# Kernel tuning notes

Hardware: AMD Instinct MI355X
Metric: run time of the kernel (lower is better)

Reference implementation:

```python
import jax, jax.numpy as jnp
import numpy as np

N_NODES = 50000
BN_EPS = 1e-5


def setup_inputs() -> dict:
    key = jax.random.key(0)
    ks = jax.random.split(key, 10)
    n, e, d, L = N_NODES, 500000, 128, 2
    x = jax.random.normal(ks[0], (n, d), dtype=jnp.float32)
    edge_index = jax.random.randint(ks[1], (2, e), 0, n, dtype=jnp.int64)
    edge_attr = jax.random.normal(ks[2], (e, d), dtype=jnp.float32)
    W1 = jax.random.normal(ks[3], (L, d, d), dtype=jnp.float32) * 0.05
    b1 = jax.random.normal(ks[4], (L, d), dtype=jnp.float32) * 0.02
    gamma = 1.0 + 0.1 * jax.random.normal(ks[5], (L, d), dtype=jnp.float32)
    beta = 0.1 * jax.random.normal(ks[6], (L, d), dtype=jnp.float32)
    W2 = jax.random.normal(ks[7], (L, d, d), dtype=jnp.float32) * 0.05
    b2 = jax.random.normal(ks[8], (L, d), dtype=jnp.float32) * 0.02
    return {"x": x, "edge_index": edge_index, "edge_attr": edge_attr,
            "W1": W1, "b1": b1, "gamma": gamma, "beta": beta, "W2": W2, "b2": b2}


def _gine_layer(x, src, dst, edge_attr, W1l, b1l, gl, bl, W2l, b2l):
    # GINEConv message: relu(x_j + edge_attr), sum-aggregated to target nodes
    msg = jax.nn.relu(x[src] + edge_attr)              # [E, d]
    agg = jax.ops.segment_sum(msg, dst, num_segments=N_NODES)  # [N, d]
    h = (x + agg) @ W1l + b1l                           # eps=0 -> (1+eps)*x = x
    # BatchNorm1d over nodes (train-mode batch stats, biased var)
    mu = jnp.mean(h, axis=0)
    var = jnp.mean(jnp.square(h - mu), axis=0)
    h = (h - mu) * jax.lax.rsqrt(var + BN_EPS) * gl + bl
    h = jax.nn.relu(h)
    h = jax.nn.relu(h @ W2l + b2l)
    return jax.nn.relu(h)  # encoder's outer activation


def reference(x, edge_index, edge_attr, W1, b1, gamma, beta, W2, b2):
    src, dst = edge_index[0], edge_index[1]
    L = W1.shape[0]
    for l in range(L):
        x = _gine_layer(x, src, dst, edge_attr, W1[l], b1[l], gamma[l], beta[l], W2[l], b2[l])
    return x
```

## Files before the change

kernel.cpp:

```cpp
#include <hip/hip_runtime.h>

#define BN_EPS 1e-5f

using f4 = __attribute__((ext_vector_type(4))) float;
using h4 = __attribute__((ext_vector_type(4))) _Float16;

__device__ inline f4 relu4(f4 v) {
    v.x = fmaxf(v.x, 0.f); v.y = fmaxf(v.y, 0.f);
    v.z = fmaxf(v.z, 0.f); v.w = fmaxf(v.w, 0.f);
    return v;
}

__global__ __launch_bounds__(256) void detect_i64_kernel(const int* __restrict__ ei,
                                                         int* __restrict__ flag, int npairs,
                                                         int* __restrict__ deg, int N) {
    __shared__ int ok;
    if (threadIdx.x == 0) ok = 1;
    __syncthreads();
    bool bad = false;
    for (int i = threadIdx.x; i < npairs; i += 256)
        bad |= (ei[2 * i + 1] != 0);
    if (bad) ok = 0;
    int nq = N >> 2;
    int4* d4 = (int4*)deg;
    for (int i = threadIdx.x; i < nq; i += 256) d4[i] = make_int4(0, 0, 0, 0);
    for (int i = (nq << 2) + threadIdx.x; i < N; i += 256) deg[i] = 0;
    __syncthreads();
    if (threadIdx.x == 0) *flag = ok;
}

__global__ __launch_bounds__(256) void canon_kernel(const int* __restrict__ ei,
                                                    const int* __restrict__ flag,
                                                    int* __restrict__ canon,
                                                    int* __restrict__ deg, int n2, int E) {
    int i = blockIdx.x * 256 + threadIdx.x;
    if (i >= n2) return;
    int wide = *flag;
    int v = wide ? ei[2 * i] : ei[i];
    canon[i] = v;
    if (i >= E) atomicAdd(&deg[v], 1);
}

__global__ __launch_bounds__(256) void scan_blk_kernel(const int* __restrict__ deg,
                                                       int* __restrict__ rowptr,
                                                       int* __restrict__ partials, int N) {
    __shared__ int s[256];
    int b = blockIdx.x, t = threadIdx.x;
    int base = b * 1024 + t * 4;
    int4 v = make_int4(0, 0, 0, 0);
    if (base + 3 < N) v = *(const int4*)(deg + base);
    else {
        if (base < N) v.x = deg[base];
        if (base + 1 < N) v.y = deg[base + 1];
        if (base + 2 < N) v.z = deg[base + 2];
        if (base + 3 < N) v.w = deg[base + 3];
    }
    s[t] = v.x + v.y + v.z + v.w;
    __syncthreads();
    for (int off = 1; off < 256; off <<= 1) {
        int u = (t >= off) ? s[t - off] : 0;
        __syncthreads();
        s[t] += u;
        __syncthreads();
    }
    int excl = (t == 0) ? 0 : s[t - 1];
    int4 w;
    w.x = excl;
    w.y = excl + v.x;
    w.z = w.y + v.y;
    w.w = w.z + v.z;
    if (base + 3 < N) *(int4*)(rowptr + base) = w;
    else {
        if (base < N) rowptr[base] = w.x;
        if (base + 1 < N) rowptr[base + 1] = w.y;
        if (base + 2 < N) rowptr[base + 2] = w.z;
        if (base + 3 < N) rowptr[base + 3] = w.w;
    }
    if (t == 255) partials[b] = s[255];
}

__global__ __launch_bounds__(256) void scan_part_kernel(int* __restrict__ partials, int nb) {
    __shared__ int s[256];
    int t = threadIdx.x;
    if (nb <= 256) {
        s[t] = (t < nb) ? partials[t] : 0;
        __syncthreads();
        for (int off = 1; off < 256; off <<= 1) {
            int u = (t >= off) ? s[t - off] : 0;
            __syncthreads();
            s[t] += u;
            __syncthreads();
        }
        if (t < nb) partials[t] = (t == 0) ? 0 : s[t - 1];
    } else if (t == 0) {
        int run = 0;
        for (int i = 0; i < nb; ++i) { int d = partials[i]; partials[i] = run; run += d; }
    }
}

__global__ __launch_bounds__(256) void scan_add_kernel(int* __restrict__ rowptr,
                                                       int* __restrict__ cursor,
                                                       const int* __restrict__ partials,
                                                       float* __restrict__ sums, int nsum,
                                                       int N, int E) {
    int i = blockIdx.x * 256 + threadIdx.x;
    if (i < nsum) sums[i] = 0.f;
    if (i < N) {
        int v = rowptr[i] + partials[i >> 10];
        rowptr[i] = v;
        cursor[i] = v;
    }
    if (i == N) rowptr[N] = E;
}

__global__ __launch_bounds__(256) void fill_kernel(const int* __restrict__ src,
                                                   const int* __restrict__ dst,
                                                   int* __restrict__ cursor,
                                                   int2* __restrict__ pbuf, int E) {
    int e = blockIdx.x * 256 + threadIdx.x;
    if (e >= E) return;
    int d = dst[e];
    int pos = atomicAdd(&cursor[d], 1);
    pbuf[pos] = make_int2(e, src[e]);
}

template <int MODE>
__global__ __launch_bounds__(256) void gather_kernel(const float* __restrict__ x,
                                                     const float* __restrict__ ea,
                                                     _Float16* __restrict__ eah,
                                                     const int* __restrict__ rowptr,
                                                     const int2* __restrict__ pbuf,
                                                     float* __restrict__ aggx, int N) {
    int t = blockIdx.x * 256 + threadIdx.x;
    int n = t >> 5;
    if (n >= N) return;
    int f = t & 31;
    int lo = rowptr[n], hi = rowptr[n + 1];
    f4 acc0 = ((const f4*)(x + (size_t)n * 128))[f];
    f4 acc1 = {0.f, 0.f, 0.f, 0.f};
    f4 acc2 = {0.f, 0.f, 0.f, 0.f};
    f4 acc3 = {0.f, 0.f, 0.f, 0.f};
    int i = lo;
    if (MODE == 1) {
        const h4* ep = (const h4*)eah;
        for (; i + 4 <= hi; i += 4) {
            int2 q0 = pbuf[i];
            int2 q1 = pbuf[i + 1];
            int2 q2 = pbuf[i + 2];
            int2 q3 = pbuf[i + 3];
            f4 xa = ((const f4*)(x + (size_t)q0.y * 128))[f];
            h4 ha = ep[(size_t)i * 32 + f];
            f4 xb = ((const f4*)(x + (size_t)q1.y * 128))[f];
            h4 hb = ep[(size_t)(i + 1) * 32 + f];
            f4 xc = ((const f4*)(x + (size_t)q2.y * 128))[f];
            h4 hc = ep[(size_t)(i + 2) * 32 + f];
            f4 xd = ((const f4*)(x + (size_t)q3.y * 128))[f];
            h4 hd = ep[(size_t)(i + 3) * 32 + f];
            acc0 += relu4(xa + __builtin_convertvector(ha, f4));
            acc1 += relu4(xb + __builtin_convertvector(hb, f4));
            acc2 += relu4(xc + __builtin_convertvector(hc, f4));
            acc3 += relu4(xd + __builtin_convertvector(hd, f4));
        }
        for (; i < hi; ++i) {
            int2 q0 = pbuf[i];
            f4 xa = ((const f4*)(x + (size_t)q0.y * 128))[f];
            h4 ha = ep[(size_t)i * 32 + f];
            acc0 += relu4(xa + __builtin_convertvector(ha, f4));
        }
    } else {
        h4* ep = (h4*)eah;
        for (; i + 4 <= hi; i += 4) {
            int2 q0 = pbuf[i];
            int2 q1 = pbuf[i + 1];
            int2 q2 = pbuf[i + 2];
            int2 q3 = pbuf[i + 3];
            f4 xa = ((const f4*)(x + (size_t)q0.y * 128))[f];
            f4 aa = __builtin_nontemporal_load(((const f4*)(ea + (size_t)q0.x * 128)) + f);
            f4 xb = ((const f4*)(x + (size_t)q1.y * 128))[f];
            f4 ab = __builtin_nontemporal_load(((const f4*)(ea + (size_t)q1.x * 128)) + f);
            f4 xc = ((const f4*)(x + (size_t)q2.y * 128))[f];
            f4 ac = __builtin_nontemporal_load(((const f4*)(ea + (size_t)q2.x * 128)) + f);
            f4 xd = ((const f4*)(x + (size_t)q3.y * 128))[f];
            f4 ad = __builtin_nontemporal_load(((const f4*)(ea + (size_t)q3.x * 128)) + f);
            if (MODE == 0) {
                ep[(size_t)i * 32 + f] = __builtin_convertvector(aa, h4);
                ep[(size_t)(i + 1) * 32 + f] = __builtin_convertvector(ab, h4);
                ep[(size_t)(i + 2) * 32 + f] = __builtin_convertvector(ac, h4);
                ep[(size_t)(i + 3) * 32 + f] = __builtin_convertvector(ad, h4);
            }
            acc0 += relu4(xa + aa);
            acc1 += relu4(xb + ab);
            acc2 += relu4(xc + ac);
            acc3 += relu4(xd + ad);
        }
        for (; i < hi; ++i) {
            int2 q0 = pbuf[i];
            f4 xa = ((const f4*)(x + (size_t)q0.y * 128))[f];
            f4 aa = __builtin_nontemporal_load(((const f4*)(ea + (size_t)q0.x * 128)) + f);
            if (MODE == 0) ep[(size_t)i * 32 + f] = __builtin_convertvector(aa, h4);
            acc0 += relu4(xa + aa);
        }
    }
    f4 r = (acc0 + acc1) + (acc2 + acc3);
    ((f4*)(aggx + (size_t)n * 128))[f] = r;
}

__global__ __launch_bounds__(256) void gemm1_kernel(const float* A,
                                                    const float* __restrict__ W,
                                                    const float* __restrict__ bias,
                                                    float* __restrict__ sums,
                                                    float* out, int N) {
    __shared__ float sA[64][132];
    __shared__ float sW[32][128];
    int t = threadIdx.x;
    int rbase = blockIdx.x * 64;

    {
        int colq = t & 31;
        int r0 = t >> 5;
#pragma unroll
        for (int it = 0; it < 8; ++it) {
            int r = r0 + it * 8;
            int row = rbase + r;
            float4 v = make_float4(0.f, 0.f, 0.f, 0.f);
            if (row < N) v = reinterpret_cast<const float4*>(A + (size_t)row * 128)[colq];
            *reinterpret_cast<float4*>(&sA[r][colq * 4]) = v;
        }
    }

    float acc[4][8];
#pragma unroll
    for (int r = 0; r < 4; ++r)
#pragma unroll
        for (int c = 0; c < 8; ++c) acc[r][c] = 0.f;

    int cg = t & 15, rg = t >> 4;
    int c0a = cg * 4;
    int c0b = 64 + cg * 4;

    for (int kc = 0; kc < 4; ++kc) {
        __syncthreads();
#pragma unroll
        for (int pass = 0; pass < 4; ++pass) {
            int kk = (t >> 5) + pass * 8;
            int k = kc * 32 + kk;
            float4 w = reinterpret_cast<const float4*>(W + (size_t)k * 128)[t & 31];
            *reinterpret_cast<float4*>(&sW[kk][(t & 31) * 4]) = w;
        }
        __syncthreads();
#pragma unroll
        for (int kk0 = 0; kk0 < 32; kk0 += 4) {
            float4 a[4];
#pragma unroll
            for (int r = 0; r < 4; ++r)
                a[r] = *reinterpret_cast<const float4*>(&sA[rg * 4 + r][kc * 32 + kk0]);
#pragma unroll
            for (int j = 0; j < 4; ++j) {
                float4 w0 = *reinterpret_cast<const float4*>(&sW[kk0 + j][c0a]);
                float4 w1 = *reinterpret_cast<const float4*>(&sW[kk0 + j][c0b]);
#pragma unroll
                for (int r = 0; r < 4; ++r) {
                    float av = (j == 0) ? a[r].x : (j == 1) ? a[r].y : (j == 2) ? a[r].z : a[r].w;
                    acc[r][0] += av * w0.x;
                    acc[r][1] += av * w0.y;
                    acc[r][2] += av * w0.z;
                    acc[r][3] += av * w0.w;
                    acc[r][4] += av * w1.x;
                    acc[r][5] += av * w1.y;
                    acc[r][6] += av * w1.z;
                    acc[r][7] += av * w1.w;
                }
            }
        }
    }

    float4 b0 = *reinterpret_cast<const float4*>(bias + c0a);
    float4 b1v = *reinterpret_cast<const float4*>(bias + c0b);
    float cs[8], cs2[8];
#pragma unroll
    for (int j = 0; j < 8; ++j) { cs[j] = 0.f; cs2[j] = 0.f; }

#pragma unroll
    for (int r = 0; r < 4; ++r) {
        int row = rbase + rg * 4 + r;
        if (row >= N) continue;
        float4 o0, o1;
        o0.x = acc[r][0] + b0.x;  o0.y = acc[r][1] + b0.y;
        o0.z = acc[r][2] + b0.z;  o0.w = acc[r][3] + b0.w;
        o1.x = acc[r][4] + b1v.x; o1.y = acc[r][5] + b1v.y;
        o1.z = acc[r][6] + b1v.z; o1.w = acc[r][7] + b1v.w;
        cs[0] += o0.x; cs2[0] += o0.x * o0.x;
        cs[1] += o0.y; cs2[1] += o0.y * o0.y;
        cs[2] += o0.z; cs2[2] += o0.z * o0.z;
        cs[3] += o0.w; cs2[3] += o0.w * o0.w;
        cs[4] += o1.x; cs2[4] += o1.x * o1.x;
        cs[5] += o1.y; cs2[5] += o1.y * o1.y;
        cs[6] += o1.z; cs2[6] += o1.z * o1.z;
        cs[7] += o1.w; cs2[7] += o1.w * o1.w;
        *reinterpret_cast<float4*>(out + (size_t)row * 128 + c0a) = o0;
        *reinterpret_cast<float4*>(out + (size_t)row * 128 + c0b) = o1;
    }

    __syncthreads();
    float* red = &sA[0][0];
    float* red2 = red + 2048;
    int base = (rg * 16 + cg) * 8;
#pragma unroll
    for (int j = 0; j < 8; ++j) { red[base + j] = cs[j]; red2[base + j] = cs2[j]; }
    __syncthreads();
    if (t < 128) {
        int cgj = (t & 63) >> 2;
        int j = (t & 3) + ((t >> 6) << 2);
        float s = 0.f, s2 = 0.f;
#pragma unroll
        for (int rr = 0; rr < 16; ++rr) {
            s += red[(rr * 16 + cgj) * 8 + j];
            s2 += red2[(rr * 16 + cgj) * 8 + j];
        }
        unsafeAtomicAdd(&sums[t], s);
        unsafeAtomicAdd(&sums[128 + t], s2);
    }
}

__global__ __launch_bounds__(256) void gemm2_kernel(const float* __restrict__ A,
                                                    const float* __restrict__ W,
                                                    const float* __restrict__ bias,
                                                    const float* __restrict__ sums,
                                                    const float* __restrict__ gamma,
                                                    const float* __restrict__ beta,
                                                    float* __restrict__ out, int N,
                                                    float invN) {
    __shared__ float sA[64][132];
    __shared__ float sW[32][128];
    __shared__ float sScale[128];
    __shared__ float sShift[128];
    int t = threadIdx.x;
    int rbase = blockIdx.x * 64;

    if (t < 128) {
        float mean = sums[t] * invN;
        float var = sums[128 + t] * invN - mean * mean;
        float inv = rsqrtf(var + BN_EPS);
        float sc = gamma[t] * inv;
        sScale[t] = sc;
        sShift[t] = beta[t] - mean * sc;
    }
    __syncthreads();

    {
        int colq = t & 31;
        int r0 = t >> 5;
        float4 s4 = reinterpret_cast<const float4*>(sScale)[colq];
        float4 sh4 = reinterpret_cast<const float4*>(sShift)[colq];
#pragma unroll
        for (int it = 0; it < 8; ++it) {
            int r = r0 + it * 8;
            int row = rbase + r;
            float4 v = make_float4(0.f, 0.f, 0.f, 0.f);
            if (row < N) {
                float4 a = reinterpret_cast<const float4*>(A + (size_t)row * 128)[colq];
                v.x = fmaxf(a.x * s4.x + sh4.x, 0.f);
                v.y = fmaxf(a.y * s4.y + sh4.y, 0.f);
                v.z = fmaxf(a.z * s4.z + sh4.z, 0.f);
                v.w = fmaxf(a.w * s4.w + sh4.w, 0.f);
            }
            *reinterpret_cast<float4*>(&sA[r][colq * 4]) = v;
        }
    }

    float acc[4][8];
#pragma unroll
    for (int r = 0; r < 4; ++r)
#pragma unroll
        for (int c = 0; c < 8; ++c) acc[r][c] = 0.f;

    int cg = t & 15, rg = t >> 4;
    int c0a = cg * 4;
    int c0b = 64 + cg * 4;

    for (int kc = 0; kc < 4; ++kc) {
        __syncthreads();
#pragma unroll
        for (int pass = 0; pass < 4; ++pass) {
            int kk = (t >> 5) + pass * 8;
            int k = kc * 32 + kk;
            float4 w = reinterpret_cast<const float4*>(W + (size_t)k * 128)[t & 31];
            *reinterpret_cast<float4*>(&sW[kk][(t & 31) * 4]) = w;
        }
        __syncthreads();
#pragma unroll
        for (int kk0 = 0; kk0 < 32; kk0 += 4) {
            float4 a[4];
#pragma unroll
            for (int r = 0; r < 4; ++r)
                a[r] = *reinterpret_cast<const float4*>(&sA[rg * 4 + r][kc * 32 + kk0]);
#pragma unroll
            for (int j = 0; j < 4; ++j) {
                float4 w0 = *reinterpret_cast<const float4*>(&sW[kk0 + j][c0a]);
                float4 w1 = *reinterpret_cast<const float4*>(&sW[kk0 + j][c0b]);
#pragma unroll
                for (int r = 0; r < 4; ++r) {
                    float av = (j == 0) ? a[r].x : (j == 1) ? a[r].y : (j == 2) ? a[r].z : a[r].w;
                    acc[r][0] += av * w0.x;
                    acc[r][1] += av * w0.y;
                    acc[r][2] += av * w0.z;
                    acc[r][3] += av * w0.w;
                    acc[r][4] += av * w1.x;
                    acc[r][5] += av * w1.y;
                    acc[r][6] += av * w1.z;
                    acc[r][7] += av * w1.w;
                }
            }
        }
    }

    float4 b0 = *reinterpret_cast<const float4*>(bias + c0a);
    float4 b1v = *reinterpret_cast<const float4*>(bias + c0b);
#pragma unroll
    for (int r = 0; r < 4; ++r) {
        int row = rbase + rg * 4 + r;
        if (row >= N) continue;
        float4 o0, o1;
        o0.x = fmaxf(acc[r][0] + b0.x, 0.f);  o0.y = fmaxf(acc[r][1] + b0.y, 0.f);
        o0.z = fmaxf(acc[r][2] + b0.z, 0.f);  o0.w = fmaxf(acc[r][3] + b0.w, 0.f);
        o1.x = fmaxf(acc[r][4] + b1v.x, 0.f); o1.y = fmaxf(acc[r][5] + b1v.y, 0.f);
        o1.z = fmaxf(acc[r][6] + b1v.z, 0.f); o1.w = fmaxf(acc[r][7] + b1v.w, 0.f);
        *reinterpret_cast<float4*>(out + (size_t)row * 128 + c0a) = o0;
        *reinterpret_cast<float4*>(out + (size_t)row * 128 + c0b) = o1;
    }
}

extern "C" void kernel_launch(void* const* d_in, const int* in_sizes, int n_in,
                              void* d_out, int out_size, void* d_ws, size_t ws_size,
                              hipStream_t stream) {
    const float* x     = (const float*)d_in[0];
    const int*   ei    = (const int*)d_in[1];
    const float* ea    = (const float*)d_in[2];
    const float* W1    = (const float*)d_in[3];
    const float* b1    = (const float*)d_in[4];
    const float* gamma = (const float*)d_in[5];
    const float* beta  = (const float*)d_in[6];
    const float* W2    = (const float*)d_in[7];
    const float* b2    = (const float*)d_in[8];

    int N = in_sizes[0] / 128;
    int E = in_sizes[2] / 128;
    int L = in_sizes[3] / (128 * 128);

    size_t NF = (size_t)N * 128;
    float*     buf    = (float*)d_ws;
    float*     sums   = buf + NF;
    _Float16*  eah    = (_Float16*)(sums + 256 * L);
    int*       canon  = (int*)(eah + (size_t)E * 128);
    int*       deg    = canon + (size_t)2 * E;
    int*       rowptr = deg + N;
    int*       cursor = rowptr + N + 2;
    int2*      pbuf   = (int2*)(cursor + N);
    int*       partials = (int*)(pbuf + E);
    int*       flag   = partials + ((N + 1023) / 1024) + 1;

    int npairs = (E < 4096) ? E : 4096;
    detect_i64_kernel<<<1, 256, 0, stream>>>(ei, flag, npairs, deg, N);
    int E2 = 2 * E;
    canon_kernel<<<(E2 + 255) / 256, 256, 0, stream>>>(ei, flag, canon, deg, E2, E);
    const int* src = canon;
    const int* dst = canon + E;

    int nb = (N + 1023) / 1024;
    scan_blk_kernel<<<nb, 256, 0, stream>>>(deg, rowptr, partials, N);
    scan_part_kernel<<<1, 256, 0, stream>>>(partials, nb);
    scan_add_kernel<<<(N + 256) / 256, 256, 0, stream>>>(rowptr, cursor, partials,
                                                         sums, 256 * L, N, E);
    int eBlocks = (E + 255) / 256;
    fill_kernel<<<eBlocks, 256, 0, stream>>>(src, dst, cursor, pbuf, E);

    int gatherBlocks = (N * 32 + 255) / 256;
    int gemmBlocks = (N + 63) / 64;
    float invN = 1.0f / (float)N;
    const float* xin = x;
    for (int l = 0; l < L; ++l) {
        float* xout = (float*)d_out;
        float* sums_l = sums + (size_t)l * 256;
        if (l == 0) {
            if (L > 1)
                gather_kernel<0><<<gatherBlocks, 256, 0, stream>>>(xin, ea, eah, rowptr,
                                                                   pbuf, buf, N);
            else
                gather_kernel<2><<<gatherBlocks, 256, 0, stream>>>(xin, ea, eah, rowptr,
                                                                   pbuf, buf, N);
        } else {
            gather_kernel<1><<<gatherBlocks, 256, 0, stream>>>(xin, ea, eah, rowptr,
                                                               pbuf, buf, N);
        }
        gemm1_kernel<<<gemmBlocks, 256, 0, stream>>>(buf, W1 + (size_t)l * 16384,
                                                     b1 + (size_t)l * 128, sums_l, buf, N);
        gemm2_kernel<<<gemmBlocks, 256, 0, stream>>>(buf, W2 + (size_t)l * 16384,
                                                     b2 + (size_t)l * 128, sums_l,
                                                     gamma + (size_t)l * 128,
                                                     beta + (size_t)l * 128, xout, N, invN);
        xin = xout;
    }
}
```

Measured before the change: 673.3 us.

## Fuse all preprocessing and layer stages into one cooperative persistent megakernel

```diff
diff --git a/kernel.cpp b/kernel.cpp
--- a/kernel.cpp
+++ b/kernel.cpp
@@ -1,4 +1,7 @@
 #include <hip/hip_runtime.h>
+#include <hip/hip_cooperative_groups.h>
+
+namespace cg = cooperative_groups;
 
 #define BN_EPS 1e-5f
 
@@ -11,300 +14,278 @@
     return v;
 }
 
-__global__ __launch_bounds__(256) void detect_i64_kernel(const int* __restrict__ ei,
-                                                         int* __restrict__ flag, int npairs,
-                                                         int* __restrict__ deg, int N) {
-    __shared__ int ok;
-    if (threadIdx.x == 0) ok = 1;
-    __syncthreads();
+struct MegaParams {
+    const float* x; const int* ei; const float* ea;
+    const float* W1; const float* b1; const float* gamma; const float* beta;
+    const float* W2; const float* b2;
+    float* out; float* buf; float* sums; _Float16* eah;
+    int* canon; int* deg; int* rowptr; int* cursor; int2* pbuf;
+    int* partials; int* flag;
+    int N, E, L, npairs;
+};
+
+__device__ inline void dev_init(int* deg, float* sums, int* flag,
+                                int N, int nsum, int gsize, int gtid) {
+    for (int i = gtid; i < N; i += gsize) deg[i] = 0;
+    for (int i = gtid; i < nsum; i += gsize) sums[i] = 0.f;
+    if (gtid == 0) *flag = 1;
+}
+
+__device__ inline void dev_detect(const int* ei, int* flag, int npairs,
+                                  int gsize, int gtid) {
     bool bad = false;
-    for (int i = threadIdx.x; i < npairs; i += 256)
-        bad |= (ei[2 * i + 1] != 0);
-    if (bad) ok = 0;
-    int nq = N >> 2;
-    int4* d4 = (int4*)deg;
-    for (int i = threadIdx.x; i < nq; i += 256) d4[i] = make_int4(0, 0, 0, 0);
-    for (int i = (nq << 2) + threadIdx.x; i < N; i += 256) deg[i] = 0;
-    __syncthreads();
-    if (threadIdx.x == 0) *flag = ok;
-}
-
-__global__ __launch_bounds__(256) void canon_kernel(const int* __restrict__ ei,
-                                                    const int* __restrict__ flag,
-                                                    int* __restrict__ canon,
-                                                    int* __restrict__ deg, int n2, int E) {
-    int i = blockIdx.x * 256 + threadIdx.x;
-    if (i >= n2) return;
+    for (int i = gtid; i < npairs; i += gsize) bad |= (ei[2 * i + 1] != 0);
+    if (bad) atomicAnd(flag, 0);
+}
+
+__device__ inline void dev_canon(const int* ei, const int* flag, int* canon,
+                                 int* deg, int n2, int E, int gsize, int gtid) {
     int wide = *flag;
-    int v = wide ? ei[2 * i] : ei[i];
-    canon[i] = v;
-    if (i >= E) atomicAdd(&deg[v], 1);
-}
-
-__global__ __launch_bounds__(256) void scan_blk_kernel(const int* __restrict__ deg,
-                                                       int* __restrict__ rowptr,
-                                                       int* __restrict__ partials, int N) {
-    __shared__ int s[256];
-    int b = blockIdx.x, t = threadIdx.x;
-    int base = b * 1024 + t * 4;
-    int4 v = make_int4(0, 0, 0, 0);
-    if (base + 3 < N) v = *(const int4*)(deg + base);
-    else {
-        if (base < N) v.x = deg[base];
-        if (base + 1 < N) v.y = deg[base + 1];
-        if (base + 2 < N) v.z = deg[base + 2];
-        if (base + 3 < N) v.w = deg[base + 3];
-    }
-    s[t] = v.x + v.y + v.z + v.w;
-    __syncthreads();
-    for (int off = 1; off < 256; off <<= 1) {
-        int u = (t >= off) ? s[t - off] : 0;
+    for (int i = gtid; i < n2; i += gsize) {
+        int v = wide ? ei[2 * i] : ei[i];
+        canon[i] = v;
+        if (i >= E) atomicAdd(deg + v, 1);
+    }
+}
+
+__device__ inline void dev_scan_local(const int* deg, int* rowptr, int* partials,
+                                      int N, int* sInt) {
+    int t = threadIdx.x;
+    int nchunks = (N + 1023) >> 10;
+    for (int c = blockIdx.x; c < (int)nchunks; c += gridDim.x) {
+        int base = (c << 10) + t * 4;
+        int4 v = make_int4(0, 0, 0, 0);
+        if (base + 3 < N) v = *(const int4*)(deg + base);
+        else {
+            if (base < N) v.x = deg[base];
+            if (base + 1 < N) v.y = deg[base + 1];
+            if (base + 2 < N) v.z = deg[base + 2];
+            if (base + 3 < N) v.w = deg[base + 3];
+        }
+        int s = v.x + v.y + v.z + v.w;
         __syncthreads();
-        s[t] += u;
-        __syncthreads();
-    }
-    int excl = (t == 0) ? 0 : s[t - 1];
-    int4 w;
-    w.x = excl;
-    w.y = excl + v.x;
-    w.z = w.y + v.y;
-    w.w = w.z + v.z;
-    if (base + 3 < N) *(int4*)(rowptr + base) = w;
-    else {
-        if (base < N) rowptr[base] = w.x;
-        if (base + 1 < N) rowptr[base + 1] = w.y;
-        if (base + 2 < N) rowptr[base + 2] = w.z;
-        if (base + 3 < N) rowptr[base + 3] = w.w;
-    }
-    if (t == 255) partials[b] = s[255];
-}
-
-__global__ __launch_bounds__(256) void scan_part_kernel(int* __restrict__ partials, int nb) {
-    __shared__ int s[256];
-    int t = threadIdx.x;
-    if (nb <= 256) {
-        s[t] = (t < nb) ? partials[t] : 0;
+        sInt[t] = s;
         __syncthreads();
         for (int off = 1; off < 256; off <<= 1) {
-            int u = (t >= off) ? s[t - off] : 0;
+            int u = (t >= off) ? sInt[t - off] : 0;
             __syncthreads();
-            s[t] += u;
+            sInt[t] += u;
             __syncthreads();
         }
-        if (t < nb) partials[t] = (t == 0) ? 0 : s[t - 1];
-    } else if (t == 0) {
+        int excl = (t == 0) ? 0 : sInt[t - 1];
+        int4 w;
+        w.x = excl;
+        w.y = excl + v.x;
+        w.z = w.y + v.y;
+        w.w = w.z + v.z;
+        if (base + 3 < N) *(int4*)(rowptr + base) = w;
+        else {
+            if (base < N) rowptr[base] = w.x;
+            if (base + 1 < N) rowptr[base + 1] = w.y;
+            if (base + 2 < N) rowptr[base + 2] = w.z;
+            if (base + 3 < N) rowptr[base + 3] = w.w;
+        }
+        if (t == 255) partials[c] = sInt[255];
+    }
+}
+
+__device__ inline void dev_scan_add(int* rowptr, int* cursor, const int* partials,
+                                    int N, int E, int* sOff, int gsize, int gtid) {
+    int nchunks = (N + 1023) >> 10;
+    if (threadIdx.x == 0) {
         int run = 0;
-        for (int i = 0; i < nb; ++i) { int d = partials[i]; partials[i] = run; run += d; }
-    }
-}
-
-__global__ __launch_bounds__(256) void scan_add_kernel(int* __restrict__ rowptr,
-                                                       int* __restrict__ cursor,
-                                                       const int* __restrict__ partials,
-                                                       float* __restrict__ sums, int nsum,
-                                                       int N, int E) {
-    int i = blockIdx.x * 256 + threadIdx.x;
-    if (i < nsum) sums[i] = 0.f;
-    if (i < N) {
-        int v = rowptr[i] + partials[i >> 10];
+        for (int c = 0; c < nchunks; ++c) { sOff[c] = run; run += partials[c]; }
+    }
+    __syncthreads();
+    for (int i = gtid; i < N; i += gsize) {
+        int v = rowptr[i] + sOff[i >> 10];
         rowptr[i] = v;
         cursor[i] = v;
     }
-    if (i == N) rowptr[N] = E;
-}
-
-__global__ __launch_bounds__(256) void fill_kernel(const int* __restrict__ src,
-                                                   const int* __restrict__ dst,
-                                                   int* __restrict__ cursor,
-                                                   int2* __restrict__ pbuf, int E) {
-    int e = blockIdx.x * 256 + threadIdx.x;
-    if (e >= E) return;
-    int d = dst[e];
-    int pos = atomicAdd(&cursor[d], 1);
-    pbuf[pos] = make_int2(e, src[e]);
-}
-
-template <int MODE>
-__global__ __launch_bounds__(256) void gather_kernel(const float* __restrict__ x,
-                                                     const float* __restrict__ ea,
-                                                     _Float16* __restrict__ eah,
-                                                     const int* __restrict__ rowptr,
-                                                     const int2* __restrict__ pbuf,
-                                                     float* __restrict__ aggx, int N) {
-    int t = blockIdx.x * 256 + threadIdx.x;
-    int n = t >> 5;
-    if (n >= N) return;
-    int f = t & 31;
-    int lo = rowptr[n], hi = rowptr[n + 1];
-    f4 acc0 = ((const f4*)(x + (size_t)n * 128))[f];
-    f4 acc1 = {0.f, 0.f, 0.f, 0.f};
-    f4 acc2 = {0.f, 0.f, 0.f, 0.f};
-    f4 acc3 = {0.f, 0.f, 0.f, 0.f};
-    int i = lo;
-    if (MODE == 1) {
-        const h4* ep = (const h4*)eah;
-        for (; i + 4 <= hi; i += 4) {
-            int2 q0 = pbuf[i];
-            int2 q1 = pbuf[i + 1];
-            int2 q2 = pbuf[i + 2];
-            int2 q3 = pbuf[i + 3];
-            f4 xa = ((const f4*)(x + (size_t)q0.y * 128))[f];
-            h4 ha = ep[(size_t)i * 32 + f];
-            f4 xb = ((const f4*)(x + (size_t)q1.y * 128))[f];
-            h4 hb = ep[(size_t)(i + 1) * 32 + f];
-            f4 xc = ((const f4*)(x + (size_t)q2.y * 128))[f];
-            h4 hc = ep[(size_t)(i + 2) * 32 + f];
-            f4 xd = ((const f4*)(x + (size_t)q3.y * 128))[f];
-            h4 hd = ep[(size_t)(i + 3) * 32 + f];
-            acc0 += relu4(xa + __builtin_convertvector(ha, f4));
-            acc1 += relu4(xb + __builtin_convertvector(hb, f4));
-            acc2 += relu4(xc + __builtin_convertvector(hc, f4));
-            acc3 += relu4(xd + __builtin_convertvector(hd, f4));
-        }
-        for (; i < hi; ++i) {
-            int2 q0 = pbuf[i];
-            f4 xa = ((const f4*)(x + (size_t)q0.y * 128))[f];
-            h4 ha = ep[(size_t)i * 32 + f];
-            acc0 += relu4(xa + __builtin_convertvector(ha, f4));
-        }
-    } else {
-        h4* ep = (h4*)eah;
-        for (; i + 4 <= hi; i += 4) {
-            int2 q0 = pbuf[i];
-            int2 q1 = pbuf[i + 1];
-            int2 q2 = pbuf[i + 2];
-            int2 q3 = pbuf[i + 3];
-            f4 xa = ((const f4*)(x + (size_t)q0.y * 128))[f];
-            f4 aa = __builtin_nontemporal_load(((const f4*)(ea + (size_t)q0.x * 128)) + f);
-            f4 xb = ((const f4*)(x + (size_t)q1.y * 128))[f];
-            f4 ab = __builtin_nontemporal_load(((const f4*)(ea + (size_t)q1.x * 128)) + f);
-            f4 xc = ((const f4*)(x + (size_t)q2.y * 128))[f];
-            f4 ac = __builtin_nontemporal_load(((const f4*)(ea + (size_t)q2.x * 128)) + f);
-            f4 xd = ((const f4*)(x + (size_t)q3.y * 128))[f];
-            f4 ad = __builtin_nontemporal_load(((const f4*)(ea + (size_t)q3.x * 128)) + f);
-            if (MODE == 0) {
-                ep[(size_t)i * 32 + f] = __builtin_convertvector(aa, h4);
-                ep[(size_t)(i + 1) * 32 + f] = __builtin_convertvector(ab, h4);
-                ep[(size_t)(i + 2) * 32 + f] = __builtin_convertvector(ac, h4);
-                ep[(size_t)(i + 3) * 32 + f] = __builtin_convertvector(ad, h4);
-            }
-            acc0 += relu4(xa + aa);
-            acc1 += relu4(xb + ab);
-            acc2 += relu4(xc + ac);
-            acc3 += relu4(xd + ad);
-        }
-        for (; i < hi; ++i) {
-            int2 q0 = pbuf[i];
-            f4 xa = ((const f4*)(x + (size_t)q0.y * 128))[f];
-            f4 aa = __builtin_nontemporal_load(((const f4*)(ea + (size_t)q0.x * 128)) + f);
-            if (MODE == 0) ep[(size_t)i * 32 + f] = __builtin_convertvector(aa, h4);
-            acc0 += relu4(xa + aa);
-        }
-    }
-    f4 r = (acc0 + acc1) + (acc2 + acc3);
-    ((f4*)(aggx + (size_t)n * 128))[f] = r;
-}
-
-__global__ __launch_bounds__(256) void gemm1_kernel(const float* A,
-                                                    const float* __restrict__ W,
-                                                    const float* __restrict__ bias,
-                                                    float* __restrict__ sums,
-                                                    float* out, int N) {
-    __shared__ float sA[64][132];
-    __shared__ float sW[32][128];
+    if (gtid == 0) rowptr[N] = E;
+}
+
+__device__ inline void dev_fill(const int* src, const int* dst, int* cursor,
+                                int2* pbuf, int E, int gsize, int gtid) {
+    for (int e = gtid; e < E; e += gsize) {
+        int d = dst[e];
+        int pos = atomicAdd(cursor + d, 1);
+        pbuf[pos] = make_int2(e, src[e]);
+    }
+}
+
+__device__ inline void dev_gather(const float* x, const float* ea, _Float16* eah,
+                                  const int* rowptr, const int2* pbuf,
+                                  float* aggx, int N, int mode,
+                                  int gid, int ngroups, int f) {
+    for (int n = gid; n < N; n += ngroups) {
+        int lo = rowptr[n], hi = rowptr[n + 1];
+        f4 acc0 = ((const f4*)(x + (size_t)n * 128))[f];
+        f4 acc1 = {0.f, 0.f, 0.f, 0.f};
+        f4 acc2 = {0.f, 0.f, 0.f, 0.f};
+        f4 acc3 = {0.f, 0.f, 0.f, 0.f};
+        int i = lo;
+        if (mode == 1) {
+            const h4* ep = (const h4*)eah;
+            for (; i + 4 <= hi; i += 4) {
+                int2 q0 = pbuf[i];
+                int2 q1 = pbuf[i + 1];
+                int2 q2 = pbuf[i + 2];
+                int2 q3 = pbuf[i + 3];
+                f4 xa = ((const f4*)(x + (size_t)q0.y * 128))[f];
+                h4 ha = ep[(size_t)i * 32 + f];
+                f4 xb = ((const f4*)(x + (size_t)q1.y * 128))[f];
+                h4 hb = ep[(size_t)(i + 1) * 32 + f];
+                f4 xc = ((const f4*)(x + (size_t)q2.y * 128))[f];
+                h4 hc = ep[(size_t)(i + 2) * 32 + f];
+                f4 xd = ((const f4*)(x + (size_t)q3.y * 128))[f];
+                h4 hd = ep[(size_t)(i + 3) * 32 + f];
+                acc0 += relu4(xa + __builtin_convertvector(ha, f4));
+                acc1 += relu4(xb + __builtin_convertvector(hb, f4));
+                acc2 += relu4(xc + __builtin_convertvector(hc, f4));
+                acc3 += relu4(xd + __builtin_convertvector(hd, f4));
+            }
+            for (; i < hi; ++i) {
+                int2 q0 = pbuf[i];
+                f4 xa = ((const f4*)(x + (size_t)q0.y * 128))[f];
+                h4 ha = ep[(size_t)i * 32 + f];
+                acc0 += relu4(xa + __builtin_convertvector(ha, f4));
+            }
+        } else {
+            h4* ep = (h4*)eah;
+            for (; i + 4 <= hi; i += 4) {
+                int2 q0 = pbuf[i];
+                int2 q1 = pbuf[i + 1];
+                int2 q2 = pbuf[i + 2];
+                int2 q3 = pbuf[i + 3];
+                f4 xa = ((const f4*)(x + (size_t)q0.y * 128))[f];
+                f4 aa = __builtin_nontemporal_load(((const f4*)(ea + (size_t)q0.x * 128)) + f);
+                f4 xb = ((const f4*)(x + (size_t)q1.y * 128))[f];
+                f4 ab = __builtin_nontemporal_load(((const f4*)(ea + (size_t)q1.x * 128)) + f);
+                f4 xc = ((const f4*)(x + (size_t)q2.y * 128))[f];
+                f4 ac = __builtin_nontemporal_load(((const f4*)(ea + (size_t)q2.x * 128)) + f);
+                f4 xd = ((const f4*)(x + (size_t)q3.y * 128))[f];
+                f4 ad = __builtin_nontemporal_load(((const f4*)(ea + (size_t)q3.x * 128)) + f);
+                if (mode == 0) {
+                    ep[(size_t)i * 32 + f] = __builtin_convertvector(aa, h4);
+                    ep[(size_t)(i + 1) * 32 + f] = __builtin_convertvector(ab, h4);
+                    ep[(size_t)(i + 2) * 32 + f] = __builtin_convertvector(ac, h4);
+                    ep[(size_t)(i + 3) * 32 + f] = __builtin_convertvector(ad, h4);
+                }
+                acc0 += relu4(xa + aa);
+                acc1 += relu4(xb + ab);
+                acc2 += relu4(xc + ac);
+                acc3 += relu4(xd + ad);
+            }
+            for (; i < hi; ++i) {
+                int2 q0 = pbuf[i];
+                f4 xa = ((const f4*)(x + (size_t)q0.y * 128))[f];
+                f4 aa = __builtin_nontemporal_load(((const f4*)(ea + (size_t)q0.x * 128)) + f);
+                if (mode == 0) ep[(size_t)i * 32 + f] = __builtin_convertvector(aa, h4);
+                acc0 += relu4(xa + aa);
+            }
+        }
+        f4 r = (acc0 + acc1) + (acc2 + acc3);
+        ((f4*)(aggx + (size_t)n * 128))[f] = r;
+    }
+}
+
+__device__ inline void dev_gemm1(const float* A, const float* W, const float* bias,
+                                 float* sums, float* out, int N,
+                                 float (*sA)[132], float (*sW)[128]) {
     int t = threadIdx.x;
-    int rbase = blockIdx.x * 64;
-
-    {
-        int colq = t & 31;
-        int r0 = t >> 5;
-#pragma unroll
-        for (int it = 0; it < 8; ++it) {
-            int r = r0 + it * 8;
-            int row = rbase + r;
-            float4 v = make_float4(0.f, 0.f, 0.f, 0.f);
-            if (row < N) v = reinterpret_cast<const float4*>(A + (size_t)row * 128)[colq];
-            *reinterpret_cast<float4*>(&sA[r][colq * 4]) = v;
-        }
-    }
-
-    float acc[4][8];
-#pragma unroll
-    for (int r = 0; r < 4; ++r)
-#pragma unroll
-        for (int c = 0; c < 8; ++c) acc[r][c] = 0.f;
-
-    int cg = t & 15, rg = t >> 4;
-    int c0a = cg * 4;
-    int c0b = 64 + cg * 4;
-
-    for (int kc = 0; kc < 4; ++kc) {
-        __syncthreads();
-#pragma unroll
-        for (int pass = 0; pass < 4; ++pass) {
-            int kk = (t >> 5) + pass * 8;
-            int k = kc * 32 + kk;
-            float4 w = reinterpret_cast<const float4*>(W + (size_t)k * 128)[t & 31];
-            *reinterpret_cast<float4*>(&sW[kk][(t & 31) * 4]) = w;
-        }
-        __syncthreads();
-#pragma unroll
-        for (int kk0 = 0; kk0 < 32; kk0 += 4) {
-            float4 a[4];
-#pragma unroll
-            for (int r = 0; r < 4; ++r)
-                a[r] = *reinterpret_cast<const float4*>(&sA[rg * 4 + r][kc * 32 + kk0]);
-#pragma unroll
-            for (int j = 0; j < 4; ++j) {
-                float4 w0 = *reinterpret_cast<const float4*>(&sW[kk0 + j][c0a]);
-                float4 w1 = *reinterpret_cast<const float4*>(&sW[kk0 + j][c0b]);
-#pragma unroll
-                for (int r = 0; r < 4; ++r) {
-                    float av = (j == 0) ? a[r].x : (j == 1) ? a[r].y : (j == 2) ? a[r].z : a[r].w;
-                    acc[r][0] += av * w0.x;
-                    acc[r][1] += av * w0.y;
-                    acc[r][2] += av * w0.z;
-                    acc[r][3] += av * w0.w;
-                    acc[r][4] += av * w1.x;
-                    acc[r][5] += av * w1.y;
-                    acc[r][6] += av * w1.z;
-                    acc[r][7] += av * w1.w;
-                }
-            }
-        }
-    }
-
+    int cgc = t & 15, rg = t >> 4;
+    int c0a = cgc * 4;
+    int c0b = 64 + cgc * 4;
     float4 b0 = *reinterpret_cast<const float4*>(bias + c0a);
     float4 b1v = *reinterpret_cast<const float4*>(bias + c0b);
     float cs[8], cs2[8];
 #pragma unroll
     for (int j = 0; j < 8; ++j) { cs[j] = 0.f; cs2[j] = 0.f; }
 
-#pragma unroll
-    for (int r = 0; r < 4; ++r) {
-        int row = rbase + rg * 4 + r;
-        if (row >= N) continue;
-        float4 o0, o1;
-        o0.x = acc[r][0] + b0.x;  o0.y = acc[r][1] + b0.y;
-        o0.z = acc[r][2] + b0.z;  o0.w = acc[r][3] + b0.w;
-        o1.x = acc[r][4] + b1v.x; o1.y = acc[r][5] + b1v.y;
-        o1.z = acc[r][6] + b1v.z; o1.w = acc[r][7] + b1v.w;
-        cs[0] += o0.x; cs2[0] += o0.x * o0.x;
-        cs[1] += o0.y; cs2[1] += o0.y * o0.y;
-        cs[2] += o0.z; cs2[2] += o0.z * o0.z;
-        cs[3] += o0.w; cs2[3] += o0.w * o0.w;
-        cs[4] += o1.x; cs2[4] += o1.x * o1.x;
-        cs[5] += o1.y; cs2[5] += o1.y * o1.y;
-        cs[6] += o1.z; cs2[6] += o1.z * o1.z;
-        cs[7] += o1.w; cs2[7] += o1.w * o1.w;
-        *reinterpret_cast<float4*>(out + (size_t)row * 128 + c0a) = o0;
-        *reinterpret_cast<float4*>(out + (size_t)row * 128 + c0b) = o1;
+    int ntiles = (N + 31) >> 5;
+    for (int tb = blockIdx.x; tb < ntiles; tb += gridDim.x) {
+        int rbase = tb << 5;
+        __syncthreads();
+        {
+            int colq = t & 31;
+            int r0 = t >> 5;
+#pragma unroll
+            for (int it = 0; it < 4; ++it) {
+                int r = r0 + it * 8;
+                int row = rbase + r;
+                float4 v = make_float4(0.f, 0.f, 0.f, 0.f);
+                if (row < N) v = reinterpret_cast<const float4*>(A + (size_t)row * 128)[colq];
+                *reinterpret_cast<float4*>(&sA[r][colq * 4]) = v;
+            }
+        }
+        float acc[2][8];
+#pragma unroll
+        for (int r = 0; r < 2; ++r)
+#pragma unroll
+            for (int c = 0; c < 8; ++c) acc[r][c] = 0.f;
+
+        for (int kc = 0; kc < 4; ++kc) {
+            __syncthreads();
+#pragma unroll
+            for (int pass = 0; pass < 4; ++pass) {
+                int kk = (t >> 5) + pass * 8;
+                int k = kc * 32 + kk;
+                float4 w = reinterpret_cast<const float4*>(W + (size_t)k * 128)[t & 31];
+                *reinterpret_cast<float4*>(&sW[kk][(t & 31) * 4]) = w;
+            }
+            __syncthreads();
+#pragma unroll
+            for (int kk0 = 0; kk0 < 32; kk0 += 4) {
+                float4 a[2];
+#pragma unroll
+                for (int r = 0; r < 2; ++r)
+                    a[r] = *reinterpret_cast<const float4*>(&sA[rg * 2 + r][kc * 32 + kk0]);
+#pragma unroll
+                for (int j = 0; j < 4; ++j) {
+                    float4 w0 = *reinterpret_cast<const float4*>(&sW[kk0 + j][c0a]);
+                    float4 w1 = *reinterpret_cast<const float4*>(&sW[kk0 + j][c0b]);
+#pragma unroll
+                    for (int r = 0; r < 2; ++r) {
+                        float av = (j == 0) ? a[r].x : (j == 1) ? a[r].y : (j == 2) ? a[r].z : a[r].w;
+                        acc[r][0] += av * w0.x;
+                        acc[r][1] += av * w0.y;
+                        acc[r][2] += av * w0.z;
+                        acc[r][3] += av * w0.w;
+                        acc[r][4] += av * w1.x;
+                        acc[r][5] += av * w1.y;
+                        acc[r][6] += av * w1.z;
+                        acc[r][7] += av * w1.w;
+                    }
+                }
+            }
+        }
+#pragma unroll
+        for (int r = 0; r < 2; ++r) {
+            int row = rbase + rg * 2 + r;
+            if (row >= N) continue;
+            float4 o0, o1;
+            o0.x = acc[r][0] + b0.x;  o0.y = acc[r][1] + b0.y;
+            o0.z = acc[r][2] + b0.z;  o0.w = acc[r][3] + b0.w;
+            o1.x = acc[r][4] + b1v.x; o1.y = acc[r][5] + b1v.y;
+            o1.z = acc[r][6] + b1v.z; o1.w = acc[r][7] + b1v.w;
+            cs[0] += o0.x; cs2[0] += o0.x * o0.x;
+            cs[1] += o0.y; cs2[1] += o0.y * o0.y;
+            cs[2] += o0.z; cs2[2] += o0.z * o0.z;
+            cs[3] += o0.w; cs2[3] += o0.w * o0.w;
+            cs[4] += o1.x; cs2[4] += o1.x * o1.x;
+            cs[5] += o1.y; cs2[5] += o1.y * o1.y;
+            cs[6] += o1.z; cs2[6] += o1.z * o1.z;
+            cs[7] += o1.w; cs2[7] += o1.w * o1.w;
+            *reinterpret_cast<float4*>(out + (size_t)row * 128 + c0a) = o0;
+            *reinterpret_cast<float4*>(out + (size_t)row * 128 + c0b) = o1;
+        }
     }
 
     __syncthreads();
     float* red = &sA[0][0];
     float* red2 = red + 2048;
-    int base = (rg * 16 + cg) * 8;
+    int base = t * 8;
 #pragma unroll
     for (int j = 0; j < 8; ++j) { red[base + j] = cs[j]; red2[base + j] = cs2[j]; }
     __syncthreads();
@@ -320,23 +301,16 @@
         unsafeAtomicAdd(&sums[t], s);
         unsafeAtomicAdd(&sums[128 + t], s2);
     }
-}
-
-__global__ __launch_bounds__(256) void gemm2_kernel(const float* __restrict__ A,
-                                                    const float* __restrict__ W,
-                                                    const float* __restrict__ bias,
-                                                    const float* __restrict__ sums,
-                                                    const float* __restrict__ gamma,
-                                                    const float* __restrict__ beta,
-                                                    float* __restrict__ out, int N,
-                                                    float invN) {
-    __shared__ float sA[64][132];
-    __shared__ float sW[32][128];
-    __shared__ float sScale[128];
-    __shared__ float sShift[128];
+    __syncthreads();
+}
+
+__device__ inline void dev_gemm2(const float* A, const float* W, const float* bias,
+                                 const float* sums, const float* gamma,
+                                 const float* beta, float* out, int N, float invN,
+                                 float (*sA)[132], float (*sW)[128],
+                                 float* sScale, float* sShift) {
     int t = threadIdx.x;
-    int rbase = blockIdx.x * 64;
-
+    __syncthreads();
     if (t < 128) {
         float mean = sums[t] * invN;
         float var = sums[128 + t] * invN - mean * mean;
@@ -347,87 +321,190 @@
     }
     __syncthreads();
 
-    {
-        int colq = t & 31;
-        int r0 = t >> 5;
-        float4 s4 = reinterpret_cast<const float4*>(sScale)[colq];
-        float4 sh4 = reinterpret_cast<const float4*>(sShift)[colq];
-#pragma unroll
-        for (int it = 0; it < 8; ++it) {
-            int r = r0 + it * 8;
-            int row = rbase + r;
-            float4 v = make_float4(0.f, 0.f, 0.f, 0.f);
-            if (row < N) {
-                float4 a = reinterpret_cast<const float4*>(A + (size_t)row * 128)[colq];
-                v.x = fmaxf(a.x * s4.x + sh4.x, 0.f);
-                v.y = fmaxf(a.y * s4.y + sh4.y, 0.f);
-                v.z = fmaxf(a.z * s4.z + sh4.z, 0.f);
-                v.w = fmaxf(a.w * s4.w + sh4.w, 0.f);
-            }
-            *reinterpret_cast<float4*>(&sA[r][colq * 4]) = v;
-        }
-    }
-
-    float acc[4][8];
-#pragma unroll
-    for (int r = 0; r < 4; ++r)
-#pragma unroll
-        for (int c = 0; c < 8; ++c) acc[r][c] = 0.f;
-
-    int cg = t & 15, rg = t >> 4;
-    int c0a = cg * 4;
-    int c0b = 64 + cg * 4;
-
-    for (int kc = 0; kc < 4; ++kc) {
-        __syncthreads();
-#pragma unroll
-        for (int pass = 0; pass < 4; ++pass) {
-            int kk = (t >> 5) + pass * 8;
-            int k = kc * 32 + kk;
-            float4 w = reinterpret_cast<const float4*>(W + (size_t)k * 128)[t & 31];
-            *reinterpret_cast<float4*>(&sW[kk][(t & 31) * 4]) = w;
-        }
-        __syncthreads();
-#pragma unroll
-        for (int kk0 = 0; kk0 < 32; kk0 += 4) {
-            float4 a[4];
-#pragma unroll
-            for (int r = 0; r < 4; ++r)
-                a[r] = *reinterpret_cast<const float4*>(&sA[rg * 4 + r][kc * 32 + kk0]);
-#pragma unroll
-            for (int j = 0; j < 4; ++j) {
-                float4 w0 = *reinterpret_cast<const float4*>(&sW[kk0 + j][c0a]);
-                float4 w1 = *reinterpret_cast<const float4*>(&sW[kk0 + j][c0b]);
-#pragma unroll
-                for (int r = 0; r < 4; ++r) {
-                    float av = (j == 0) ? a[r].x : (j == 1) ? a[r].y : (j == 2) ? a[r].z : a[r].w;
-                    acc[r][0] += av * w0.x;
-                    acc[r][1] += av * w0.y;
-                    acc[r][2] += av * w0.z;
-                    acc[r][3] += av * w0.w;
-                    acc[r][4] += av * w1.x;
-                    acc[r][5] += av * w1.y;
-                    acc[r][6] += av * w1.z;
-                    acc[r][7] += av * w1.w;
-                }
-            }
-        }
-    }
-
+    int cgc = t & 15, rg = t >> 4;
+    int c0a = cgc * 4;
+    int c0b = 64 + cgc * 4;
     float4 b0 = *reinterpret_cast<const float4*>(bias + c0a);
     float4 b1v = *reinterpret_cast<const float4*>(bias + c0b);
-#pragma unroll
-    for (int r = 0; r < 4; ++r) {
-        int row = rbase + rg * 4 + r;
-        if (row >= N) continue;
-        float4 o0, o1;
-        o0.x = fmaxf(acc[r][0] + b0.x, 0.f);  o0.y = fmaxf(acc[r][1] + b0.y, 0.f);
-        o0.z = fmaxf(acc[r][2] + b0.z, 0.f);  o0.w = fmaxf(acc[r][3] + b0.w, 0.f);
-        o1.x = fmaxf(acc[r][4] + b1v.x, 0.f); o1.y = fmaxf(acc[r][5] + b1v.y, 0.f);
-        o1.z = fmaxf(acc[r][6] + b1v.z, 0.f); o1.w = fmaxf(acc[r][7] + b1v.w, 0.f);
-        *reinterpret_cast<float4*>(out + (size_t)row * 128 + c0a) = o0;
-        *reinterpret_cast<float4*>(out + (size_t)row * 128 + c0b) = o1;
-    }
+
+    int ntiles = (N + 31) >> 5;
+    for (int tb = blockIdx.x; tb < ntiles; tb += gridDim.x) {
+        int rbase = tb << 5;
+        __syncthreads();
+        {
+            int colq = t & 31;
+            int r0 = t >> 5;
+            float4 s4 = reinterpret_cast<const float4*>(sScale)[colq];
+            float4 sh4 = reinterpret_cast<const float4*>(sShift)[colq];
+#pragma unroll
+            for (int it = 0; it < 4; ++it) {
+                int r = r0 + it * 8;
+                int row = rbase + r;
+                float4 v = make_float4(0.f, 0.f, 0.f, 0.f);
+                if (row < N) {
+                    float4 a = reinterpret_cast<const float4*>(A + (size_t)row * 128)[colq];
+                    v.x = fmaxf(a.x * s4.x + sh4.x, 0.f);
+                    v.y = fmaxf(a.y * s4.y + sh4.y, 0.f);
+                    v.z = fmaxf(a.z * s4.z + sh4.z, 0.f);
+                    v.w = fmaxf(a.w * s4.w + sh4.w, 0.f);
+                }
+                *reinterpret_cast<float4*>(&sA[r][colq * 4]) = v;
+            }
+        }
+        float acc[2][8];
+#pragma unroll
+        for (int r = 0; r < 2; ++r)
+#pragma unroll
+            for (int c = 0; c < 8; ++c) acc[r][c] = 0.f;
+
+        for (int kc = 0; kc < 4; ++kc) {
+            __syncthreads();
+#pragma unroll
+            for (int pass = 0; pass < 4; ++pass) {
+                int kk = (t >> 5) + pass * 8;
+                int k = kc * 32 + kk;
+                float4 w = reinterpret_cast<const float4*>(W + (size_t)k * 128)[t & 31];
+                *reinterpret_cast<float4*>(&sW[kk][(t & 31) * 4]) = w;
+            }
+            __syncthreads();
+#pragma unroll
+            for (int kk0 = 0; kk0 < 32; kk0 += 4) {
+                float4 a[2];
+#pragma unroll
+                for (int r = 0; r < 2; ++r)
+                    a[r] = *reinterpret_cast<const float4*>(&sA[rg * 2 + r][kc * 32 + kk0]);
+#pragma unroll
+                for (int j = 0; j < 4; ++j) {
+                    float4 w0 = *reinterpret_cast<const float4*>(&sW[kk0 + j][c0a]);
+                    float4 w1 = *reinterpret_cast<const float4*>(&sW[kk0 + j][c0b]);
+#pragma unroll
+                    for (int r = 0; r < 2; ++r) {
+                        float av = (j == 0) ? a[r].x : (j == 1) ? a[r].y : (j == 2) ? a[r].z : a[r].w;
+                        acc[r][0] += av * w0.x;
+                        acc[r][1] += av * w0.y;
+                        acc[r][2] += av * w0.z;
+                        acc[r][3] += av * w0.w;
+                        acc[r][4] += av * w1.x;
+                        acc[r][5] += av * w1.y;
+                        acc[r][6] += av * w1.z;
+                        acc[r][7] += av * w1.w;
+                    }
+                }
+            }
+        }
+#pragma unroll
+        for (int r = 0; r < 2; ++r) {
+            int row = rbase + rg * 2 + r;
+            if (row >= N) continue;
+            float4 o0, o1;
+            o0.x = fmaxf(acc[r][0] + b0.x, 0.f);  o0.y = fmaxf(acc[r][1] + b0.y, 0.f);
+            o0.z = fmaxf(acc[r][2] + b0.z, 0.f);  o0.w = fmaxf(acc[r][3] + b0.w, 0.f);
+            o1.x = fmaxf(acc[r][4] + b1v.x, 0.f); o1.y = fmaxf(acc[r][5] + b1v.y, 0.f);
+            o1.z = fmaxf(acc[r][6] + b1v.z, 0.f); o1.w = fmaxf(acc[r][7] + b1v.w, 0.f);
+            *reinterpret_cast<float4*>(out + (size_t)row * 128 + c0a) = o0;
+            *reinterpret_cast<float4*>(out + (size_t)row * 128 + c0b) = o1;
+        }
+    }
+    __syncthreads();
+}
+
+__global__ __launch_bounds__(256, 4) void mega_kernel(MegaParams p) {
+    cg::grid_group grid = cg::this_grid();
+    __shared__ float sA[32][132];
+    __shared__ float sW[32][128];
+    __shared__ float sScale[128];
+    __shared__ float sShift[128];
+    __shared__ int sOff[128];
+
+    int t = threadIdx.x;
+    int gtid = blockIdx.x * 256 + t;
+    int gsize = gridDim.x * 256;
+
+    dev_init(p.deg, p.sums, p.flag, p.N, 256 * p.L, gsize, gtid);
+    grid.sync();
+    dev_detect(p.ei, p.flag, p.npairs, gsize, gtid);
+    grid.sync();
+    dev_canon(p.ei, p.flag, p.canon, p.deg, 2 * p.E, p.E, gsize, gtid);
+    grid.sync();
+    dev_scan_local(p.deg, p.rowptr, p.partials, p.N, (int*)&sA[0][0]);
+    grid.sync();
+    dev_scan_add(p.rowptr, p.cursor, p.partials, p.N, p.E, sOff, gsize, gtid);
+    grid.sync();
+    dev_fill(p.canon, p.canon + p.E, p.cursor, p.pbuf, p.E, gsize, gtid);
+    grid.sync();
+
+    int gid = gtid >> 5;
+    int ngroups = gsize >> 5;
+    int f = t & 31;
+    float invN = 1.0f / (float)p.N;
+    const float* xin = p.x;
+    for (int l = 0; l < p.L; ++l) {
+        int mode = (l == 0) ? ((p.L > 1) ? 0 : 2) : 1;
+        dev_gather(xin, p.ea, p.eah, p.rowptr, p.pbuf, p.buf, p.N, mode, gid, ngroups, f);
+        grid.sync();
+        dev_gemm1(p.buf, p.W1 + (size_t)l * 16384, p.b1 + (size_t)l * 128,
+                  p.sums + (size_t)l * 256, p.buf, p.N, sA, sW);
+        grid.sync();
+        dev_gemm2(p.buf, p.W2 + (size_t)l * 16384, p.b2 + (size_t)l * 128,
+                  p.sums + (size_t)l * 256, p.gamma + (size_t)l * 128,
+                  p.beta + (size_t)l * 128, p.out, p.N, invN, sA, sW, sScale, sShift);
+        grid.sync();
+        xin = p.out;
+    }
+}
+
+__global__ __launch_bounds__(256) void fb_init_kernel(int* deg, float* sums, int* flag,
+                                                      int N, int nsum) {
+    int gtid = blockIdx.x * 256 + threadIdx.x;
+    int gsize = gridDim.x * 256;
+    dev_init(deg, sums, flag, N, nsum, gsize, gtid);
+}
+__global__ __launch_bounds__(256) void fb_detect_kernel(const int* ei, int* flag, int npairs) {
+    dev_detect(ei, flag, npairs, gridDim.x * 256, blockIdx.x * 256 + threadIdx.x);
+}
+__global__ __launch_bounds__(256) void fb_canon_kernel(const int* ei, const int* flag,
+                                                       int* canon, int* deg, int n2, int E) {
+    dev_canon(ei, flag, canon, deg, n2, E, gridDim.x * 256, blockIdx.x * 256 + threadIdx.x);
+}
+__global__ __launch_bounds__(256) void fb_scan_local_kernel(const int* deg, int* rowptr,
+                                                            int* partials, int N) {
+    __shared__ int sInt[256];
+    dev_scan_local(deg, rowptr, partials, N, sInt);
+}
+__global__ __launch_bounds__(256) void fb_scan_add_kernel(int* rowptr, int* cursor,
+                                                          const int* partials, int N, int E) {
+    __shared__ int sOff[128];
+    dev_scan_add(rowptr, cursor, partials, N, E, sOff,
+                 gridDim.x * 256, blockIdx.x * 256 + threadIdx.x);
+}
+__global__ __launch_bounds__(256) void fb_fill_kernel(const int* src, const int* dst,
+                                                      int* cursor, int2* pbuf, int E) {
+    dev_fill(src, dst, cursor, pbuf, E, gridDim.x * 256, blockIdx.x * 256 + threadIdx.x);
+}
+__global__ __launch_bounds__(256) void fb_gather_kernel(const float* x, const float* ea,
+                                                        _Float16* eah, const int* rowptr,
+                                                        const int2* pbuf, float* aggx,
+                                                        int N, int mode) {
+    int gtid = blockIdx.x * 256 + threadIdx.x;
+    dev_gather(x, ea, eah, rowptr, pbuf, aggx, N, mode,
+               gtid >> 5, (gridDim.x * 256) >> 5, threadIdx.x & 31);
+}
+__global__ __launch_bounds__(256) void fb_gemm1_kernel(const float* A, const float* W,
+                                                       const float* bias, float* sums,
+                                                       float* out, int N) {
+    __shared__ float sA[32][132];
+    __shared__ float sW[32][128];
+    dev_gemm1(A, W, bias, sums, out, N, sA, sW);
+}
+__global__ __launch_bounds__(256) void fb_gemm2_kernel(const float* A, const float* W,
+                                                       const float* bias, const float* sums,
+                                                       const float* gamma, const float* beta,
+                                                       float* out, int N, float invN) {
+    __shared__ float sA[32][132];
+    __shared__ float sW[32][128];
+    __shared__ float sScale[128];
+    __shared__ float sShift[128];
+    dev_gemm2(A, W, bias, sums, gamma, beta, out, N, invN, sA, sW, sScale, sShift);
 }
 
 extern "C" void kernel_launch(void* const* d_in, const int* in_sizes, int n_in,
@@ -460,44 +537,67 @@
     int*       flag   = partials + ((N + 1023) / 1024) + 1;
 
     int npairs = (E < 4096) ? E : 4096;
-    detect_i64_kernel<<<1, 256, 0, stream>>>(ei, flag, npairs, deg, N);
-    int E2 = 2 * E;
-    canon_kernel<<<(E2 + 255) / 256, 256, 0, stream>>>(ei, flag, canon, deg, E2, E);
-    const int* src = canon;
-    const int* dst = canon + E;
-
-    int nb = (N + 1023) / 1024;
-    scan_blk_kernel<<<nb, 256, 0, stream>>>(deg, rowptr, partials, N);
-    scan_part_kernel<<<1, 256, 0, stream>>>(partials, nb);
-    scan_add_kernel<<<(N + 256) / 256, 256, 0, stream>>>(rowptr, cursor, partials,
-                                                         sums, 256 * L, N, E);
-    int eBlocks = (E + 255) / 256;
-    fill_kernel<<<eBlocks, 256, 0, stream>>>(src, dst, cursor, pbuf, E);
-
-    int gatherBlocks = (N * 32 + 255) / 256;
-    int gemmBlocks = (N + 63) / 64;
-    float invN = 1.0f / (float)N;
-    const float* xin = x;
-    for (int l = 0; l < L; ++l) {
-        float* xout = (float*)d_out;
-        float* sums_l = sums + (size_t)l * 256;
-        if (l == 0) {
-            if (L > 1)
-                gather_kernel<0><<<gatherBlocks, 256, 0, stream>>>(xin, ea, eah, rowptr,
-                                                                   pbuf, buf, N);
-            else
-                gather_kernel<2><<<gatherBlocks, 256, 0, stream>>>(xin, ea, eah, rowptr,
-                                                                   pbuf, buf, N);
-        } else {
-            gather_kernel<1><<<gatherBlocks, 256, 0, stream>>>(xin, ea, eah, rowptr,
-                                                               pbuf, buf, N);
-        }
-        gemm1_kernel<<<gemmBlocks, 256, 0, stream>>>(buf, W1 + (size_t)l * 16384,
-                                                     b1 + (size_t)l * 128, sums_l, buf, N);
-        gemm2_kernel<<<gemmBlocks, 256, 0, stream>>>(buf, W2 + (size_t)l * 16384,
-                                                     b2 + (size_t)l * 128, sums_l,
-                                                     gamma + (size_t)l * 128,
-                                                     beta + (size_t)l * 128, xout, N, invN);
-        xin = xout;
-    }
-}
+
+    static int coopBlocks = -1;
+    if (coopBlocks < 0) {
+        int nb = 0;
+        hipError_t e1 = hipOccupancyMaxActiveBlocksPerMultiprocessor(&nb, mega_kernel, 256, 0);
+        hipDeviceProp_t prop{};
+        hipError_t e2 = hipGetDeviceProperties(&prop, 0);
+        if (e1 == hipSuccess && e2 == hipSuccess && nb > 0 && prop.multiProcessorCount > 0)
+            coopBlocks = nb * prop.multiProcessorCount;
+        else
+            coopBlocks = 0;
+        if (coopBlocks > 4096) coopBlocks = 4096;
+    }
+
+    bool launched = false;
+    if (coopBlocks > 0) {
+        MegaParams p;
+        p.x = x; p.ei = ei; p.ea = ea;
+        p.W1 = W1; p.b1 = b1; p.gamma = gamma; p.beta = beta;
+        p.W2 = W2; p.b2 = b2;
+        p.out = (float*)d_out; p.buf = buf; p.sums = sums; p.eah = eah;
+        p.canon = canon; p.deg = deg; p.rowptr = rowptr; p.cursor = cursor;
+        p.pbuf = pbuf; p.partials = partials; p.flag = flag;
+        p.N = N; p.E = E; p.L = L; p.npairs = npairs;
+        void* args[] = { (void*)&p };
+        hipError_t rc = hipLaunchCooperativeKernel((const void*)mega_kernel,
+                                                   dim3(coopBlocks), dim3(256),
+                                                   args, 0, stream);
+        launched = (rc == hipSuccess);
+    }
+
+    if (!launched) {
+        int gridS = 2048;
+        fb_init_kernel<<<(N + 255) / 256, 256, 0, stream>>>(deg, sums, flag, N, 256 * L);
+        fb_detect_kernel<<<1, 256, 0, stream>>>(ei, flag, npairs);
+        int E2 = 2 * E;
+        fb_canon_kernel<<<(E2 + 255) / 256, 256, 0, stream>>>(ei, flag, canon, deg, E2, E);
+        int nb2 = (N + 1023) / 1024;
+        fb_scan_local_kernel<<<nb2, 256, 0, stream>>>(deg, rowptr, partials, N);
+        fb_scan_add_kernel<<<(N + 256) / 256, 256, 0, stream>>>(rowptr, cursor, partials, N, E);
+        fb_fill_kernel<<<(E + 255) / 256, 256, 0, stream>>>(canon, canon + E, cursor, pbuf, E);
+        int gatherBlocks = (N * 32 + 255) / 256;
+        int gemmBlocks = (N + 31) / 32;
+        if (gemmBlocks > gridS) gemmBlocks = gridS;
+        float invN = 1.0f / (float)N;
+        const float* xin = x;
+        for (int l = 0; l < L; ++l) {
+            float* xout = (float*)d_out;
+            float* sums_l = sums + (size_t)l * 256;
+            int mode = (l == 0) ? ((L > 1) ? 0 : 2) : 1;
+            fb_gather_kernel<<<gatherBlocks, 256, 0, stream>>>(xin, ea, eah, rowptr,
+                                                               pbuf, buf, N, mode);
+            fb_gemm1_kernel<<<gemmBlocks, 256, 0, stream>>>(buf, W1 + (size_t)l * 16384,
+                                                            b1 + (size_t)l * 128, sums_l,
+                                                            buf, N);
+            fb_gemm2_kernel<<<gemmBlocks, 256, 0, stream>>>(buf, W2 + (size_t)l * 16384,
+                                                            b2 + (size_t)l * 128, sums_l,
+                                                            gamma + (size_t)l * 128,
+                                                            beta + (size_t)l * 128,
+                                                            xout, N, invN);
+            xin = xout;
+        }
+    }
+}
```

New measurement: 867.0 us. +28.8%, slower.
